# Kernel optimization log

Measured on AMD Instinct MI355X. Metric: run time of the kernel, lower is better.

## Reference

```python
import jax, jax.numpy as jnp
import numpy as np

B, C, D, H = 128, 8, 1024, 8
K_RANGE = (2, 3, 4, 5)


def setup_inputs() -> dict:
    key = jax.random.key(0)
    ks = jax.random.split(key, 10)
    s = 0.02
    return {
        "x": jax.random.normal(ks[0], (B, D), jnp.float32),
        # per-K prototype groups, shape (nb_classes, K, embed_dim) as in get_prototype_group()
        "p2": jax.random.normal(ks[1], (C, 2, D), jnp.float32),
        "p3": jax.random.normal(ks[2], (C, 3, D), jnp.float32),
        "p4": jax.random.normal(ks[3], (C, 4, D), jnp.float32),
        "p5": jax.random.normal(ks[4], (C, 5, D), jnp.float32),
        # per-class attention Block params (stacked over class axis)
        "ln_g": jnp.ones((C, D), jnp.float32),
        "ln_b": jnp.zeros((C, D), jnp.float32),
        "w_qkv": jax.random.normal(ks[5], (C, 3 * D, D), jnp.float32) * s,
        "b_qkv": jnp.zeros((C, 3 * D), jnp.float32),
        "w_proj": jax.random.normal(ks[6], (C, D, D), jnp.float32) * s,
        "b_proj": jnp.zeros((C, D), jnp.float32),
        # cls head
        "w_cls": jax.random.normal(ks[7], (C, D), jnp.float32) * s,
        "b_cls": jnp.zeros((C,), jnp.float32),
    }


def _proto_group(x, pg):
    """x: (B,D); pg: (C,K,D). Returns nearest proto (B,D), per-sample class group (B,K,D), class ids (B,)."""
    Cc, K, d = pg.shape
    flat = pg.reshape(Cc * K, d)
    # squared L2 distances (argmin identical to torch.cdist p=2 argmin)
    d2 = (jnp.sum(x * x, axis=1, keepdims=True)
          - 2.0 * (x @ flat.T)
          + jnp.sum(flat * flat, axis=1))
    idx = jnp.argmin(d2, axis=1)          # (B,)
    cls = idx // K                        # (B,)
    return flat[idx], pg[cls], cls


def _vicreg(x, nearest, proto_space, sim_c=25.0, std_c=25.0, cov_c=1.0):
    # sim: pull x toward its nearest prototype in every K-group
    repr_loss = jnp.mean((x[:, None, :] - nearest) ** 2)
    # std over batch of prototype space, unbiased var, eps=1e-4
    std = jnp.sqrt(jnp.var(proto_space, axis=0, ddof=1) + 1e-4)   # (S,D)
    std_loss = jnp.mean(jax.nn.relu(1.0 - std))
    # covariance of centered flattened prototype space
    ps = proto_space - jnp.mean(proto_space, axis=0)
    P = ps.reshape(-1, ps.shape[-1])                              # (B*S, D)
    cov = P.T @ P / (P.shape[0] - 1)
    cov_loss = ((cov ** 2).sum() - (jnp.diagonal(cov) ** 2).sum()) / ps.shape[-1]
    return sim_c * repr_loss + std_c * std_loss + cov_c * cov_loss


def _forward(x, p2, p3, p4, p5, ln_g, ln_b, w_qkv, b_qkv, w_proj, b_proj, w_cls, b_cls):
    groups = (p2, p3, p4, p5)
    nearest_list, space_list, cls = [], [], None
    for pg in groups:
        n, sp, cls = _proto_group(x, pg)   # cls kept from LAST group, as in torch code
        nearest_list.append(n)
        space_list.append(sp)
    nearest = jnp.stack(nearest_list, axis=1)     # (B, len(K_range), D)
    proto_space = jnp.concatenate(space_list, 1)  # (B, sum(K_range), D)

    vcr = _vicreg(x, nearest, proto_space)

    # per-class attention Block: LayerNorm -> MHA -> residual, vectorized over class axis c
    S = proto_space.shape[1]
    mu = proto_space.mean(-1, keepdims=True)
    var = proto_space.var(-1, keepdims=True)
    xn = (proto_space - mu) * jax.lax.rsqrt(var + 1e-5)               # (B,S,D)
    h = xn[None] * ln_g[:, None, None, :] + ln_b[:, None, None, :]    # (C,B,S,D)

    qkv = jnp.einsum('cbsd,cfd->cbsf', h, w_qkv) + b_qkv[:, None, None, :]
    dh = D // H
    qkv = qkv.reshape(C, B, S, 3, H, dh).transpose(3, 0, 1, 4, 2, 5)  # (3,C,B,H,S,dh)
    q, k, v = qkv[0] * (dh ** -0.5), qkv[1], qkv[2]
    attn = jax.nn.softmax(jnp.einsum('cbhqe,cbhke->cbhqk', q, k), axis=-1)
    o = jnp.einsum('cbhqk,cbhke->cbhqe', attn, v)                     # (C,B,H,S,dh)
    o = o.transpose(0, 1, 3, 2, 4).reshape(C, B, S, D)
    out = jnp.einsum('cbsd,ced->cbse', o, w_proj) + b_proj[:, None, None, :]
    attended = proto_space[None] + out                                # (C,B,S,D)

    # route each sample through the block of its (last-group) assigned class
    cond = attended[cls, jnp.arange(B)]                               # (B,S,D)
    cond = cond / jnp.maximum(jnp.linalg.norm(cond, axis=2, keepdims=True), 1e-12)
    pooled = cond.mean(1)                                             # (B,D)
    logits = pooled @ w_cls.T + b_cls
    return logits, vcr


def reference(x, p2, p3, p4, p5, ln_g, ln_b, w_qkv, b_qkv, w_proj, b_proj, w_cls, b_cls):
    return _forward(x, p2, p3, p4, p5, ln_g, ln_b, w_qkv, b_qkv, w_proj, b_proj, w_cls, b_cls)
```

## Files before the change

### kernel.cpp

```cpp
#include <hip/hip_runtime.h>
#include <math.h>

#define NB 128
#define ND 1024
#define NS 14
#define NDH 128

typedef float f32x4 __attribute__((ext_vector_type(4)));
typedef short bf16x8 __attribute__((ext_vector_type(8)));
typedef unsigned int u32x4 __attribute__((ext_vector_type(4)));

__device__ __forceinline__ unsigned short f2bf(float v) {
  unsigned int u = __builtin_bit_cast(unsigned int, v);
  return (unsigned short)((u + 0x7FFFu + ((u >> 16) & 1u)) >> 16);
}
__device__ __forceinline__ float bf2f(unsigned short u) {
  return __builtin_bit_cast(float, (unsigned int)u << 16);
}

__device__ __forceinline__ bf16x8 pack_bv(float4 w0, float4 w1) {
  unsigned int u0, u1, u2, u3;
  asm("v_cvt_pk_bf16_f32 %0, %1, %2" : "=v"(u0) : "v"(w0.x), "v"(w0.y));
  asm("v_cvt_pk_bf16_f32 %0, %1, %2" : "=v"(u1) : "v"(w0.z), "v"(w0.w));
  asm("v_cvt_pk_bf16_f32 %0, %1, %2" : "=v"(u2) : "v"(w1.x), "v"(w1.y));
  asm("v_cvt_pk_bf16_f32 %0, %1, %2" : "=v"(u3) : "v"(w1.z), "v"(w1.w));
  u32x4 u = {u0, u1, u2, u3};
  return __builtin_bit_cast(bf16x8, u);
}

__device__ __forceinline__ void s_decomp(int s, int& g, int& k) {
  if (s < 2)      { g = 0; k = s; }
  else if (s < 5) { g = 1; k = s - 2; }
  else if (s < 9) { g = 2; k = s - 5; }
  else            { g = 3; k = s - 9; }
}
__device__ __forceinline__ const float* grp_ptr(int g, const float* p2, const float* p3,
                                                const float* p4, const float* p5) {
  return g == 0 ? p2 : g == 1 ? p3 : g == 2 ? p4 : p5;
}
__device__ __forceinline__ int grp_base(int g) { return g == 0 ? 0 : g == 1 ? 16 : g == 2 ? 40 : 72; }
__device__ __forceinline__ int grp_k(int g) { return g + 2; }

__global__ __launch_bounds__(256) void k_ln(
    const float* __restrict__ p2, const float* __restrict__ p3,
    const float* __restrict__ p4, const float* __restrict__ p5,
    const float* __restrict__ ln_g, const float* __restrict__ ln_b,
    unsigned short* __restrict__ hbf2, float* __restrict__ pall)
{
  int r = blockIdx.x, t = threadIdx.x;
  __shared__ __align__(16) float xs[ND];
  float4* xs4 = (float4*)xs;
  const float* pp; int idx;
  if (r < 16)      { pp = p2; idx = r; }
  else if (r < 40) { pp = p3; idx = r - 16; }
  else if (r < 72) { pp = p4; idx = r - 40; }
  else             { pp = p5; idx = r - 72; }
  const float4* row4 = (const float4*)(pp + (size_t)idx * ND);
  float4 v = row4[t];
  xs4[t] = v;
  float s1 = v.x + v.y + v.z + v.w;
  float s2 = v.x * v.x + v.y * v.y + v.z * v.z + v.w * v.w;
  __shared__ float ra[256], rb[256];
  ra[t] = s1; rb[t] = s2; __syncthreads();
  for (int o = 128; o > 0; o >>= 1) { if (t < o) { ra[t] += ra[t + o]; rb[t] += rb[t + o]; } __syncthreads(); }
  __shared__ float mu, rstd;
  if (t == 0) {
    float m = ra[0] * (1.f / 1024.f);
    float var = rb[0] * (1.f / 1024.f) - m * m;
    mu = m; rstd = rsqrtf(var + 1e-5f);
  }
  __syncthreads();
  ((float4*)(pall + (size_t)r * ND))[t] = xs4[t];
  float4 xv = xs4[t];
  float nx = (xv.x - mu) * rstd, ny = (xv.y - mu) * rstd,
        nz = (xv.z - mu) * rstd, nw = (xv.w - mu) * rstd;
  int d0 = t * 4;
  int m = r >> 4, rr = r & 15;
  int kblk = d0 >> 5, qq = (d0 >> 3) & 3, e0 = d0 & 7;
  size_t fidx = (size_t)kblk * 3584 + m * 512 + (qq * 16 + rr) * 8 + e0;
#pragma unroll
  for (int c = 0; c < 8; ++c) {
    float4 g = ((const float4*)(ln_g + (size_t)c * ND))[t];
    float4 bb = ((const float4*)(ln_b + (size_t)c * ND))[t];
    ushort4 u;
    u.x = f2bf(nx * g.x + bb.x); u.y = f2bf(ny * g.y + bb.y);
    u.z = f2bf(nz * g.z + bb.z); u.w = f2bf(nw * g.w + bb.w);
    *(ushort4*)&hbf2[(size_t)c * 114688 + fidx] = u;
  }
}

__global__ __launch_bounds__(512) void k_qkv_assign(
    const unsigned short* __restrict__ hbf2, const float* __restrict__ w_qkv,
    const float* __restrict__ b_qkv, unsigned short* __restrict__ qkv_bf,
    const float* __restrict__ x,
    const float* __restrict__ p2, const float* __restrict__ p3,
    const float* __restrict__ p4, const float* __restrict__ p5,
    int* __restrict__ cls, int* __restrict__ rows_g, float* __restrict__ minv)
{
  __shared__ __align__(16) float lred[3 * 2 * 7 * 256];
  int bid = blockIdx.x, t = threadIdx.x;
  if (bid < 768) {
    int c = bid / 96, xb = bid - c * 96;
    int lane = t & 63, wid = t >> 6;
    int cg = wid & 1, ks = wid >> 1;
    int r16 = lane & 15, q = lane >> 4;
    int col = xb * 32 + cg * 16 + r16;
    const float* Wp = w_qkv + ((size_t)c * 3072 + col) * ND + ks * 256 + q * 8;
    const unsigned short* Hp = hbf2 + (size_t)c * 114688 + (size_t)(ks * 8) * 3584 + lane * 8;
    f32x4 acc[7] = {};
#pragma unroll
    for (int i = 0; i < 8; ++i) {
      float4 w0 = *(const float4*)(Wp + i * 32);
      float4 w1 = *(const float4*)(Wp + i * 32 + 4);
      bf16x8 bv = pack_bv(w0, w1);
      const unsigned short* hk = Hp + (size_t)i * 3584;
#pragma unroll
      for (int m = 0; m < 7; ++m) {
        bf16x8 av = *(const bf16x8*)(hk + m * 512);
        acc[m] = __builtin_amdgcn_mfma_f32_16x16x32_bf16(av, bv, acc[m], 0, 0, 0);
      }
    }
    if (ks) {
#pragma unroll
      for (int m = 0; m < 7; ++m)
        *(f32x4*)&lred[(((ks - 1) * 2 + cg) * 7 + m) * 256 + lane * 4] = acc[m];
    }
    __syncthreads();
    if (ks == 0) {
      float bq = b_qkv[(size_t)c * 3072 + col];
#pragma unroll
      for (int m = 0; m < 7; ++m) {
        f32x4 a1 = *(const f32x4*)&lred[((0 * 2 + cg) * 7 + m) * 256 + lane * 4];
        f32x4 a2 = *(const f32x4*)&lred[((1 * 2 + cg) * 7 + m) * 256 + lane * 4];
        f32x4 a3 = *(const f32x4*)&lred[((2 * 2 + cg) * 7 + m) * 256 + lane * 4];
#pragma unroll
        for (int r = 0; r < 4; ++r) {
          int row = m * 16 + q * 4 + r;
          qkv_bf[((size_t)c * 112 + row) * 3072 + col] = f2bf(acc[m][r] + a1[r] + a2[r] + a3[r] + bq);
        }
      }
    }
  } else {
    int b = bid - 768;
    float4* xs4 = (float4*)lred;
    float* d2s = lred + 1024;
    int* cls_s = (int*)(lred + 1152);
    if (t < 256) {
      const float4* xg4 = (const float4*)(x + (size_t)b * ND);
      xs4[t] = xg4[t];
    }
    __syncthreads();
    if (t < 112) {
      const float* pp; int idx;
      if (t < 16)      { pp = p2; idx = t; }
      else if (t < 40) { pp = p3; idx = t - 16; }
      else if (t < 72) { pp = p4; idx = t - 40; }
      else             { pp = p5; idx = t - 72; }
      const float4* pr4 = (const float4*)(pp + (size_t)idx * ND);
      float acc = 0.f;
#pragma unroll 8
      for (int d = 0; d < 256; ++d) {
        float4 a = xs4[d], p = pr4[d];
        float dx = a.x - p.x, dy = a.y - p.y, dz = a.z - p.z, dw = a.w - p.w;
        acc += dx * dx + dy * dy + dz * dz + dw * dw;
      }
      d2s[t] = acc;
    }
    __syncthreads();
    if (t < 4) {
      int base = grp_base(t), kg = grp_k(t), cnt = 8 * kg;
      float mv = d2s[base]; int mi = 0;
      for (int j = 1; j < cnt; ++j) { float v = d2s[base + j]; if (v < mv) { mv = v; mi = j; } }
      int c = mi / kg;
      cls[b * 4 + t] = c; cls_s[t] = c;
      minv[b * 4 + t] = mv;
    }
    __syncthreads();
    if (t < NS) {
      int g, k; s_decomp(t, g, k);
      rows_g[b * NS + t] = grp_base(g) + cls_s[g] * grp_k(g) + k;
    }
  }
}

__global__ __launch_bounds__(128) void k_prep(
    const int* __restrict__ cls, const float* __restrict__ minv,
    int* __restrict__ counts, int* __restrict__ ccnt, int* __restrict__ order,
    int* __restrict__ posof, int* __restrict__ chunkidx, int* __restrict__ chunk_c,
    int* __restrict__ chunk_lo, int* __restrict__ chunkN, float* __restrict__ scal)
{
  __shared__ int cnt_s[32];
  __shared__ int cc_s[8];
  __shared__ float red[128];
  int t = threadIdx.x;
  if (t < 32) cnt_s[t] = 0;
  if (t < 8) cc_s[t] = 0;
  if (t < 4) scal[t] = 0.f;
  __syncthreads();
  int c3;
#pragma unroll
  for (int g = 0; g < 4; ++g) {
    int c = cls[t * 4 + g];
    atomicAdd(&cnt_s[g * 8 + c], 1);
    if (g == 3) c3 = c;
  }
  int pos = atomicAdd(&cc_s[c3], 1);
  order[c3 * 128 + pos] = t;
  posof[t] = pos;
  red[t] = minv[t * 4 + 0] + minv[t * 4 + 1] + minv[t * 4 + 2] + minv[t * 4 + 3];
  __syncthreads();
  for (int o = 64; o > 0; o >>= 1) { if (t < o) red[t] += red[t + o]; __syncthreads(); }
  if (t == 0) {
    scal[0] = red[0];
    int T = 0;
    for (int c = 0; c < 8; ++c) {
      chunkidx[c] = T;
      int nch = (cc_s[c] + 15) >> 4;
      for (int j = 0; j < nch; ++j) { chunk_c[T] = c; chunk_lo[T] = j * 16; ++T; }
    }
    chunkN[0] = T;
  }
  if (t < 32) counts[t] = cnt_s[t];
  if (t < 8) ccnt[t] = cc_s[t];
}

__global__ __launch_bounds__(256) void k_attn_stats(
    const unsigned short* __restrict__ qkv_bf, const int* __restrict__ cls,
    const int* __restrict__ rows_g, const int* __restrict__ posof,
    const int* __restrict__ chunkidx, unsigned short* __restrict__ obf2,
    const float* __restrict__ p2, const float* __restrict__ p3,
    const float* __restrict__ p4, const float* __restrict__ p5,
    const int* __restrict__ counts, float* __restrict__ M, float* __restrict__ scal)
{
  int bid = blockIdx.x, t = threadIdx.x;
  if (bid < 1024) {
    __shared__ __align__(16) float qs[NS * NDH], ks2[NS * NDH], vs[NS * NDH];
    __shared__ float sc[NS * NS];
    __shared__ int rg[NS];
    int h = bid & 7, b = bid >> 3;
    if (t < NS) rg[t] = rows_g[b * NS + t];
    __syncthreads();
    int cp = cls[b * 4 + 3];
    int pos = posof[b];
    size_t gbase = (size_t)(chunkidx[cp] + (pos >> 4)) * 229376;
    int slot = pos & 15;
    const float scale = 0.08838834764831843f;
    for (int i = t; i < NS * 32; i += 256) {
      int s = i >> 5, e4 = (i & 31) * 4;
      size_t base = ((size_t)cp * 112 + rg[s]) * 3072 + h * NDH + e4;
      ushort4 uq = *(const ushort4*)&qkv_bf[base];
      ushort4 uk = *(const ushort4*)&qkv_bf[base + 1024];
      ushort4 uv = *(const ushort4*)&qkv_bf[base + 2048];
      int o = s * NDH + e4;
      qs[o]     = bf2f(uq.x) * scale; qs[o + 1] = bf2f(uq.y) * scale;
      qs[o + 2] = bf2f(uq.z) * scale; qs[o + 3] = bf2f(uq.w) * scale;
      ks2[o]     = bf2f(uk.x); ks2[o + 1] = bf2f(uk.y);
      ks2[o + 2] = bf2f(uk.z); ks2[o + 3] = bf2f(uk.w);
      vs[o]     = bf2f(uv.x); vs[o + 1] = bf2f(uv.y);
      vs[o + 2] = bf2f(uv.z); vs[o + 3] = bf2f(uv.w);
    }
    __syncthreads();
    if (t < NS * NS) {
      int si = t / NS, sj = t - (t / NS) * NS;
      const float4* qa = (const float4*)&qs[si * NDH];
      const float4* kb = (const float4*)&ks2[sj * NDH];
      float acc = 0.f;
#pragma unroll 8
      for (int e4 = 0; e4 < 32; ++e4) {
        float4 a = qa[e4], k4 = kb[e4];
        acc += a.x * k4.x + a.y * k4.y + a.z * k4.z + a.w * k4.w;
      }
      sc[t] = acc;
    }
    __syncthreads();
    if (t < NS) {
      float mx = -1e30f;
      for (int j = 0; j < NS; ++j) mx = fmaxf(mx, sc[t * NS + j]);
      float e_[NS]; float sum = 0.f;
      for (int j = 0; j < NS; ++j) { float e = expf(sc[t * NS + j] - mx); e_[j] = e; sum += e; }
      float inv = 1.f / sum;
      for (int j = 0; j < NS; ++j) sc[t * NS + j] = e_[j] * inv;
    }
    __syncthreads();
    for (int i = t; i < NS * 32; i += 256) {
      int s = i >> 5, e4 = i & 31;
      float4 a = {0.f, 0.f, 0.f, 0.f};
#pragma unroll
      for (int j = 0; j < NS; ++j) {
        float w = sc[s * NS + j];
        float4 v4 = ((const float4*)&vs[j * NDH])[e4];
        a.x += w * v4.x; a.y += w * v4.y; a.z += w * v4.z; a.w += w * v4.w;
      }
      int row = slot * 14 + s;
      int m = row >> 4, r16 = row & 15;
      int d0 = h * NDH + e4 * 4;
      int kblk = d0 >> 5, qq = (d0 >> 3) & 3, e0 = d0 & 7;
      ushort4 u; u.x = f2bf(a.x); u.y = f2bf(a.y); u.z = f2bf(a.z); u.w = f2bf(a.w);
      *(ushort4*)&obf2[gbase + (size_t)kblk * 7168 + m * 512 + (qq * 16 + r16) * 8 + e0] = u;
    }
  } else {
    int idx = (bid - 1024) * 256 + t;
    int s = idx >> 10, d = idx & 1023;
    int g, k; s_decomp(s, g, k);
    const float* pp = grp_ptr(g, p2, p3, p4, p5);
    int kg = grp_k(g);
    float vc[8], nc[8];
    float sum = 0.f, sumsq = 0.f;
#pragma unroll
    for (int c = 0; c < 8; ++c) {
      float v = pp[((size_t)(c * kg + k)) * ND + d];
      float n = (float)counts[g * 8 + c];
      vc[c] = v; nc[c] = n;
      sum += n * v; sumsq += n * v * v;
    }
    float mean = sum * (1.f / 128.f);
    float var = (sumsq - 128.f * mean * mean) * (1.f / 127.f);
    float sd = sqrtf(var + 1e-4f);
#pragma unroll
    for (int c = 0; c < 8; ++c)
      M[((size_t)(s * 8 + c)) * ND + d] = sqrtf(nc[c] * (1.f / 1791.f)) * (vc[c] - mean);
    float part = fmaxf(1.f - sd, 0.f);
    __shared__ float red[256];
    red[t] = part; __syncthreads();
    for (int o = 128; o > 0; o >>= 1) { if (t < o) red[t] += red[t + o]; __syncthreads(); }
    if (t == 0) atomicAdd(&scal[1], red[0]);
  }
}

__global__ __launch_bounds__(512) void k_proj_gram(
    const unsigned short* __restrict__ obf2, const int* __restrict__ order,
    const int* __restrict__ ccnt, const int* __restrict__ chunk_c,
    const int* __restrict__ chunk_lo, const int* __restrict__ chunkN,
    const int* __restrict__ rows_g,
    const float* __restrict__ w_proj, const float* __restrict__ b_proj,
    const float* __restrict__ pall, float* __restrict__ att,
    const float* __restrict__ M, float* __restrict__ scal)
{
  int bid = blockIdx.x, t = threadIdx.x;
  if (bid < 960) {
    int g = bid / 64, xb = bid - g * 64;
    if (g >= chunkN[0]) return;
    __shared__ __align__(16) float lred[3 * 2 * 7 * 256];
    __shared__ int sid_s[16];
    int c = chunk_c[g], lo = chunk_lo[g];
    int cnt = ccnt[c];
    int nb = cnt - lo; if (nb > 16) nb = 16;
    int lane = t & 63, wid = t >> 6;
    int rh = wid & 1, ks = wid >> 1;
    if (t < 16) sid_s[t] = order[c * 128 + lo + ((t < nb) ? t : nb - 1)];
    int r16 = lane & 15, q = lane >> 4;
    int col = xb * 16 + r16;
    const float* Wp = w_proj + ((size_t)c * ND + col) * ND + ks * 256 + q * 8;
    const unsigned short* Ap = obf2 + (size_t)g * 229376 + (size_t)(ks * 8) * 7168 + rh * 3584 + lane * 8;
    f32x4 acc[7] = {};
#pragma unroll
    for (int i = 0; i < 8; ++i) {
      float4 w0 = *(const float4*)(Wp + i * 32);
      float4 w1 = *(const float4*)(Wp + i * 32 + 4);
      bf16x8 bv = pack_bv(w0, w1);
      const unsigned short* ak = Ap + (size_t)i * 7168;
#pragma unroll
      for (int m = 0; m < 7; ++m) {
        bf16x8 av = *(const bf16x8*)(ak + m * 512);
        acc[m] = __builtin_amdgcn_mfma_f32_16x16x32_bf16(av, bv, acc[m], 0, 0, 0);
      }
    }
    if (ks) {
#pragma unroll
      for (int m = 0; m < 7; ++m)
        *(f32x4*)&lred[(((ks - 1) * 2 + rh) * 7 + m) * 256 + lane * 4] = acc[m];
    }
    __syncthreads();
    if (ks == 0) {
      float bp = b_proj[(size_t)c * ND + col];
#pragma unroll
      for (int m = 0; m < 7; ++m) {
        f32x4 a1 = *(const f32x4*)&lred[((0 * 2 + rh) * 7 + m) * 256 + lane * 4];
        f32x4 a2 = *(const f32x4*)&lred[((1 * 2 + rh) * 7 + m) * 256 + lane * 4];
        f32x4 a3 = *(const f32x4*)&lred[((2 * 2 + rh) * 7 + m) * 256 + lane * 4];
#pragma unroll
        for (int r = 0; r < 4; ++r) {
          int row = rh * 112 + m * 16 + q * 4 + r;
          int slot = row / 14, s = row - slot * 14;
          if (slot < nb) {
            int b = sid_s[slot];
            float res = pall[(size_t)rows_g[b * NS + s] * ND + col];
            att[((size_t)b * NS + s) * ND + col] = acc[m][r] + a1[r] + a2[r] + a3[r] + bp + res;
          }
        }
      }
    }
  } else if (bid < 1072) {
    int r = bid - 960;
    __shared__ __align__(16) float mi[ND];
    __shared__ float red2[128];
    float4* mi4 = (float4*)mi;
    const float4* src4 = (const float4*)(M + (size_t)r * ND);
    if (t < 256) mi4[t] = src4[t];
    if (t < 128) red2[t] = 0.f;
    __syncthreads();
    int j = t >> 2, qd = t & 3;
    float p = 0.f;
    if (j < 112) {
      const float4* mj4 = (const float4*)(M + (size_t)j * ND);
      float acc = 0.f;
#pragma unroll 8
      for (int d = qd * 64; d < qd * 64 + 64; ++d) {
        float4 a = mi4[d], b = mj4[d];
        acc += a.x * b.x + a.y * b.y + a.z * b.z + a.w * b.w;
      }
      acc += __shfl_xor(acc, 1, 4);
      acc += __shfl_xor(acc, 2, 4);
      p = acc * acc;
    }
    if (qd == 0 && j < 112) red2[j] = p;
    __syncthreads();
    for (int o = 64; o > 0; o >>= 1) { if (t < o) red2[t] += red2[t + o]; __syncthreads(); }
    if (t == 0) atomicAdd(&scal[2], red2[0]);
  } else {
    int d = (bid - 1072) * 512 + t;
    float tsum = 0.f;
    for (int r = 0; r < 112; ++r) { float v = M[(size_t)r * ND + d]; tsum += v * v; }
    __shared__ float red3[512];
    red3[t] = tsum * tsum; __syncthreads();
    for (int o = 256; o > 0; o >>= 1) { if (t < o) red3[t] += red3[t + o]; __syncthreads(); }
    if (t == 0) atomicAdd(&scal[3], red3[0]);
  }
}

__global__ __launch_bounds__(256) void k_final(
    const float* __restrict__ att, const float* __restrict__ w_cls,
    const float* __restrict__ b_cls, const float* __restrict__ scal,
    float* __restrict__ out)
{
  int b = blockIdx.x, t = threadIdx.x;
  __shared__ __align__(16) float as[NS * ND];
  __shared__ float wred[NS][4];
  __shared__ float inv[NS];
  __shared__ __align__(16) float pooled[ND];
  int lane = t & 63, w = t >> 6;
#pragma unroll
  for (int s = 0; s < NS; ++s) {
    float4 v = ((const float4*)(att + ((size_t)b * NS + s) * ND))[t];
    ((float4*)&as[s * ND])[t] = v;
    float p = v.x * v.x + v.y * v.y + v.z * v.z + v.w * v.w;
#pragma unroll
    for (int o = 32; o > 0; o >>= 1) p += __shfl_xor(p, o, 64);
    if (lane == 0) wred[s][w] = p;
  }
  __syncthreads();
  if (t < NS) {
    float s2 = wred[t][0] + wred[t][1] + wred[t][2] + wred[t][3];
    inv[t] = 1.f / fmaxf(sqrtf(s2), 1e-12f);
  }
  __syncthreads();
  float4 pa = {0.f, 0.f, 0.f, 0.f};
#pragma unroll
  for (int s = 0; s < NS; ++s) {
    float iv = inv[s];
    float4 v = ((const float4*)&as[s * ND])[t];
    pa.x += iv * v.x; pa.y += iv * v.y; pa.z += iv * v.z; pa.w += iv * v.w;
  }
  const float k14 = 1.f / 14.f;
  pa.x *= k14; pa.y *= k14; pa.z *= k14; pa.w *= k14;
  ((float4*)pooled)[t] = pa;
  __syncthreads();
  int c = t >> 5, l = t & 31;
  float acc = 0.f;
#pragma unroll
  for (int k = 0; k < 8; ++k) {
    int i4 = l + k * 32;
    float4 p4 = ((const float4*)pooled)[i4];
    float4 wc = ((const float4*)(w_cls + (size_t)c * ND))[i4];
    acc += p4.x * wc.x + p4.y * wc.y + p4.z * wc.z + p4.w * wc.w;
  }
  for (int o = 16; o > 0; o >>= 1) acc += __shfl_down(acc, o, 32);
  if (l == 0) out[b * 8 + c] = acc + b_cls[c];
  if (b == 0 && t == 0) {
    float repr = scal[0] * (1.f / (128.f * 4.f * 1024.f));
    float stdl = scal[1] * (1.f / 14336.f);
    float covl = (scal[2] - scal[3]) * (1.f / 1024.f);
    out[1024] = 25.f * repr + 25.f * stdl + covl;
  }
}

extern "C" void kernel_launch(void* const* d_in, const int* in_sizes, int n_in,
                              void* d_out, int out_size, void* d_ws, size_t ws_size,
                              hipStream_t stream) {
  const float* x      = (const float*)d_in[0];
  const float* p2     = (const float*)d_in[1];
  const float* p3     = (const float*)d_in[2];
  const float* p4     = (const float*)d_in[3];
  const float* p5     = (const float*)d_in[4];
  const float* ln_g   = (const float*)d_in[5];
  const float* ln_b   = (const float*)d_in[6];
  const float* w_qkv  = (const float*)d_in[7];
  const float* b_qkv  = (const float*)d_in[8];
  const float* w_proj = (const float*)d_in[9];
  const float* b_proj = (const float*)d_in[10];
  const float* w_cls  = (const float*)d_in[11];
  const float* b_cls  = (const float*)d_in[12];
  float* out = (float*)d_out;
  char* ws = (char*)d_ws;

  float* scal      = (float*)(ws + 0);
  int*   counts    = (int*)(ws + 64);
  int*   ccnt      = (int*)(ws + 192);
  int*   cls       = (int*)(ws + 256);
  int*   rows_g    = (int*)(ws + 2304);
  int*   order     = (int*)(ws + 9472);
  float* minv      = (float*)(ws + 13568);
  int*   posof     = (int*)(ws + 15616);
  int*   chunkidx  = (int*)(ws + 16128);
  int*   chunk_c   = (int*)(ws + 16160);
  int*   chunk_lo  = (int*)(ws + 16224);
  int*   chunkN    = (int*)(ws + 16288);
  float* pall      = (float*)(ws + 16384);
  unsigned short* hbf2 = (unsigned short*)(ws + 475136);
  unsigned short* qkvb = (unsigned short*)(ws + 2310144);
  unsigned short* obf2 = (unsigned short*)(ws + 7815168);
  float* att       = (float*)(ws + 15155200);
  float* M         = (float*)(ws + 22495232);

  k_ln<<<112, 256, 0, stream>>>(p2, p3, p4, p5, ln_g, ln_b, hbf2, pall);
  k_qkv_assign<<<896, 512, 0, stream>>>(hbf2, w_qkv, b_qkv, qkvb,
                                        x, p2, p3, p4, p5, cls, rows_g, minv);
  k_prep<<<1, 128, 0, stream>>>(cls, minv, counts, ccnt, order, posof, chunkidx, chunk_c, chunk_lo, chunkN, scal);
  k_attn_stats<<<1080, 256, 0, stream>>>(qkvb, cls, rows_g, posof, chunkidx, obf2,
                                         p2, p3, p4, p5, counts, M, scal);
  k_proj_gram<<<1074, 512, 0, stream>>>(obf2, order, ccnt, chunk_c, chunk_lo, chunkN, rows_g,
                                        w_proj, b_proj, pall, att, M, scal);
  k_final<<<128, 256, 0, stream>>>(att, w_cls, b_cls, scal, out);
}
```

Before: 124.0 us.

## Regroup stages into fewer kernels, halve GEMM blocks, prefetch MFMA operands

```diff
diff --git a/kernel.cpp b/kernel.cpp
--- a/kernel.cpp
+++ b/kernel.cpp
@@ -41,136 +41,87 @@
 __device__ __forceinline__ int grp_base(int g) { return g == 0 ? 0 : g == 1 ? 16 : g == 2 ? 40 : 72; }
 __device__ __forceinline__ int grp_k(int g) { return g + 2; }
 
-__global__ __launch_bounds__(256) void k_ln(
+__global__ __launch_bounds__(256) void k_ln_assign(
+    const float* __restrict__ x,
     const float* __restrict__ p2, const float* __restrict__ p3,
     const float* __restrict__ p4, const float* __restrict__ p5,
     const float* __restrict__ ln_g, const float* __restrict__ ln_b,
-    unsigned short* __restrict__ hbf2, float* __restrict__ pall)
+    unsigned short* __restrict__ hbf2, float* __restrict__ pall,
+    int* __restrict__ cls, int* __restrict__ rows_g, float* __restrict__ minv)
 {
-  int r = blockIdx.x, t = threadIdx.x;
+  int bid = blockIdx.x, t = threadIdx.x;
   __shared__ __align__(16) float xs[ND];
   float4* xs4 = (float4*)xs;
-  const float* pp; int idx;
-  if (r < 16)      { pp = p2; idx = r; }
-  else if (r < 40) { pp = p3; idx = r - 16; }
-  else if (r < 72) { pp = p4; idx = r - 40; }
-  else             { pp = p5; idx = r - 72; }
-  const float4* row4 = (const float4*)(pp + (size_t)idx * ND);
-  float4 v = row4[t];
-  xs4[t] = v;
-  float s1 = v.x + v.y + v.z + v.w;
-  float s2 = v.x * v.x + v.y * v.y + v.z * v.z + v.w * v.w;
-  __shared__ float ra[256], rb[256];
-  ra[t] = s1; rb[t] = s2; __syncthreads();
-  for (int o = 128; o > 0; o >>= 1) { if (t < o) { ra[t] += ra[t + o]; rb[t] += rb[t + o]; } __syncthreads(); }
-  __shared__ float mu, rstd;
-  if (t == 0) {
-    float m = ra[0] * (1.f / 1024.f);
-    float var = rb[0] * (1.f / 1024.f) - m * m;
-    mu = m; rstd = rsqrtf(var + 1e-5f);
-  }
-  __syncthreads();
-  ((float4*)(pall + (size_t)r * ND))[t] = xs4[t];
-  float4 xv = xs4[t];
-  float nx = (xv.x - mu) * rstd, ny = (xv.y - mu) * rstd,
-        nz = (xv.z - mu) * rstd, nw = (xv.w - mu) * rstd;
-  int d0 = t * 4;
-  int m = r >> 4, rr = r & 15;
-  int kblk = d0 >> 5, qq = (d0 >> 3) & 3, e0 = d0 & 7;
-  size_t fidx = (size_t)kblk * 3584 + m * 512 + (qq * 16 + rr) * 8 + e0;
-#pragma unroll
-  for (int c = 0; c < 8; ++c) {
-    float4 g = ((const float4*)(ln_g + (size_t)c * ND))[t];
-    float4 bb = ((const float4*)(ln_b + (size_t)c * ND))[t];
-    ushort4 u;
-    u.x = f2bf(nx * g.x + bb.x); u.y = f2bf(ny * g.y + bb.y);
-    u.z = f2bf(nz * g.z + bb.z); u.w = f2bf(nw * g.w + bb.w);
-    *(ushort4*)&hbf2[(size_t)c * 114688 + fidx] = u;
-  }
-}
-
-__global__ __launch_bounds__(512) void k_qkv_assign(
-    const unsigned short* __restrict__ hbf2, const float* __restrict__ w_qkv,
-    const float* __restrict__ b_qkv, unsigned short* __restrict__ qkv_bf,
-    const float* __restrict__ x,
-    const float* __restrict__ p2, const float* __restrict__ p3,
-    const float* __restrict__ p4, const float* __restrict__ p5,
-    int* __restrict__ cls, int* __restrict__ rows_g, float* __restrict__ minv)
-{
-  __shared__ __align__(16) float lred[3 * 2 * 7 * 256];
-  int bid = blockIdx.x, t = threadIdx.x;
-  if (bid < 768) {
-    int c = bid / 96, xb = bid - c * 96;
-    int lane = t & 63, wid = t >> 6;
-    int cg = wid & 1, ks = wid >> 1;
-    int r16 = lane & 15, q = lane >> 4;
-    int col = xb * 32 + cg * 16 + r16;
-    const float* Wp = w_qkv + ((size_t)c * 3072 + col) * ND + ks * 256 + q * 8;
-    const unsigned short* Hp = hbf2 + (size_t)c * 114688 + (size_t)(ks * 8) * 3584 + lane * 8;
-    f32x4 acc[7] = {};
-#pragma unroll
-    for (int i = 0; i < 8; ++i) {
-      float4 w0 = *(const float4*)(Wp + i * 32);
-      float4 w1 = *(const float4*)(Wp + i * 32 + 4);
-      bf16x8 bv = pack_bv(w0, w1);
-      const unsigned short* hk = Hp + (size_t)i * 3584;
-#pragma unroll
-      for (int m = 0; m < 7; ++m) {
-        bf16x8 av = *(const bf16x8*)(hk + m * 512);
-        acc[m] = __builtin_amdgcn_mfma_f32_16x16x32_bf16(av, bv, acc[m], 0, 0, 0);
-      }
-    }
-    if (ks) {
-#pragma unroll
-      for (int m = 0; m < 7; ++m)
-        *(f32x4*)&lred[(((ks - 1) * 2 + cg) * 7 + m) * 256 + lane * 4] = acc[m];
-    }
-    __syncthreads();
-    if (ks == 0) {
-      float bq = b_qkv[(size_t)c * 3072 + col];
-#pragma unroll
-      for (int m = 0; m < 7; ++m) {
-        f32x4 a1 = *(const f32x4*)&lred[((0 * 2 + cg) * 7 + m) * 256 + lane * 4];
-        f32x4 a2 = *(const f32x4*)&lred[((1 * 2 + cg) * 7 + m) * 256 + lane * 4];
-        f32x4 a3 = *(const f32x4*)&lred[((2 * 2 + cg) * 7 + m) * 256 + lane * 4];
-#pragma unroll
-        for (int r = 0; r < 4; ++r) {
-          int row = m * 16 + q * 4 + r;
-          qkv_bf[((size_t)c * 112 + row) * 3072 + col] = f2bf(acc[m][r] + a1[r] + a2[r] + a3[r] + bq);
-        }
-      }
+  if (bid < 112) {
+    int r = bid;
+    const float* pp; int idx;
+    if (r < 16)      { pp = p2; idx = r; }
+    else if (r < 40) { pp = p3; idx = r - 16; }
+    else if (r < 72) { pp = p4; idx = r - 40; }
+    else             { pp = p5; idx = r - 72; }
+    const float4* row4 = (const float4*)(pp + (size_t)idx * ND);
+    float4 v = row4[t];
+    xs4[t] = v;
+    float s1 = v.x + v.y + v.z + v.w;
+    float s2 = v.x * v.x + v.y * v.y + v.z * v.z + v.w * v.w;
+    __shared__ float ra[256], rb[256];
+    ra[t] = s1; rb[t] = s2; __syncthreads();
+    for (int o = 128; o > 0; o >>= 1) { if (t < o) { ra[t] += ra[t + o]; rb[t] += rb[t + o]; } __syncthreads(); }
+    __shared__ float mu, rstd;
+    if (t == 0) {
+      float m = ra[0] * (1.f / 1024.f);
+      float var = rb[0] * (1.f / 1024.f) - m * m;
+      mu = m; rstd = rsqrtf(var + 1e-5f);
+    }
+    __syncthreads();
+    ((float4*)(pall + (size_t)r * ND))[t] = xs4[t];
+    float4 xv = xs4[t];
+    float nx = (xv.x - mu) * rstd, ny = (xv.y - mu) * rstd,
+          nz = (xv.z - mu) * rstd, nw = (xv.w - mu) * rstd;
+    int d0 = t * 4;
+    int m = r >> 4, rr = r & 15;
+    int kblk = d0 >> 5, qq = (d0 >> 3) & 3, e0 = d0 & 7;
+    size_t fidx = (size_t)kblk * 3584 + m * 512 + (qq * 16 + rr) * 8 + e0;
+#pragma unroll
+    for (int c = 0; c < 8; ++c) {
+      float4 g = ((const float4*)(ln_g + (size_t)c * ND))[t];
+      float4 bb = ((const float4*)(ln_b + (size_t)c * ND))[t];
+      ushort4 u;
+      u.x = f2bf(nx * g.x + bb.x); u.y = f2bf(ny * g.y + bb.y);
+      u.z = f2bf(nz * g.z + bb.z); u.w = f2bf(nw * g.w + bb.w);
+      *(ushort4*)&hbf2[(size_t)c * 114688 + fidx] = u;
     }
   } else {
-    int b = bid - 768;
-    float4* xs4 = (float4*)lred;
-    float* d2s = lred + 1024;
-    int* cls_s = (int*)(lred + 1152);
-    if (t < 256) {
-      const float4* xg4 = (const float4*)(x + (size_t)b * ND);
-      xs4[t] = xg4[t];
-    }
-    __syncthreads();
-    if (t < 112) {
+    int b = bid - 112;
+    __shared__ float d2s[112];
+    __shared__ int cls_s[4];
+    const float4* xg4 = (const float4*)(x + (size_t)b * ND);
+    xs4[t] = xg4[t];
+    __syncthreads();
+    int j = t >> 1, half = t & 1;
+    if (j < 112) {
       const float* pp; int idx;
-      if (t < 16)      { pp = p2; idx = t; }
-      else if (t < 40) { pp = p3; idx = t - 16; }
-      else if (t < 72) { pp = p4; idx = t - 40; }
-      else             { pp = p5; idx = t - 72; }
+      if (j < 16)      { pp = p2; idx = j; }
+      else if (j < 40) { pp = p3; idx = j - 16; }
+      else if (j < 72) { pp = p4; idx = j - 40; }
+      else             { pp = p5; idx = j - 72; }
       const float4* pr4 = (const float4*)(pp + (size_t)idx * ND);
       float acc = 0.f;
+      int d0 = half * 128;
 #pragma unroll 8
-      for (int d = 0; d < 256; ++d) {
+      for (int d = d0; d < d0 + 128; ++d) {
         float4 a = xs4[d], p = pr4[d];
         float dx = a.x - p.x, dy = a.y - p.y, dz = a.z - p.z, dw = a.w - p.w;
         acc += dx * dx + dy * dy + dz * dz + dw * dw;
       }
-      d2s[t] = acc;
+      acc += __shfl_xor(acc, 1, 2);
+      if (half == 0) d2s[j] = acc;
     }
     __syncthreads();
     if (t < 4) {
       int base = grp_base(t), kg = grp_k(t), cnt = 8 * kg;
       float mv = d2s[base]; int mi = 0;
-      for (int j = 1; j < cnt; ++j) { float v = d2s[base + j]; if (v < mv) { mv = v; mi = j; } }
+      for (int jj = 1; jj < cnt; ++jj) { float v = d2s[base + jj]; if (v < mv) { mv = v; mi = jj; } }
       int c = mi / kg;
       cls[b * 4 + t] = c; cls_s[t] = c;
       minv[b * 4 + t] = mv;
@@ -183,45 +134,105 @@
   }
 }
 
-__global__ __launch_bounds__(128) void k_prep(
+__global__ __launch_bounds__(256, 4) void k_qkv_prep(
+    const unsigned short* __restrict__ hbf2, const float* __restrict__ w_qkv,
+    const float* __restrict__ b_qkv, unsigned short* __restrict__ qkv_bf,
     const int* __restrict__ cls, const float* __restrict__ minv,
     int* __restrict__ counts, int* __restrict__ ccnt, int* __restrict__ order,
     int* __restrict__ posof, int* __restrict__ chunkidx, int* __restrict__ chunk_c,
     int* __restrict__ chunk_lo, int* __restrict__ chunkN, float* __restrict__ scal)
 {
-  __shared__ int cnt_s[32];
-  __shared__ int cc_s[8];
-  __shared__ float red[128];
-  int t = threadIdx.x;
-  if (t < 32) cnt_s[t] = 0;
-  if (t < 8) cc_s[t] = 0;
-  if (t < 4) scal[t] = 0.f;
+  int bid = blockIdx.x, t = threadIdx.x;
+  if (bid == 0) {
+    __shared__ int cnt_s[32];
+    __shared__ int cc_s[8];
+    __shared__ float red[128];
+    if (t < 32) cnt_s[t] = 0;
+    if (t < 8) cc_s[t] = 0;
+    if (t < 4) scal[t] = 0.f;
+    __syncthreads();
+    if (t < 128) {
+      int c3;
+#pragma unroll
+      for (int g = 0; g < 4; ++g) {
+        int c = cls[t * 4 + g];
+        atomicAdd(&cnt_s[g * 8 + c], 1);
+        if (g == 3) c3 = c;
+      }
+      int pos = atomicAdd(&cc_s[c3], 1);
+      order[c3 * 128 + pos] = t;
+      posof[t] = pos;
+      red[t] = minv[t * 4 + 0] + minv[t * 4 + 1] + minv[t * 4 + 2] + minv[t * 4 + 3];
+    }
+    __syncthreads();
+    for (int o = 64; o > 0; o >>= 1) { if (t < o) red[t] += red[t + o]; __syncthreads(); }
+    if (t == 0) {
+      scal[0] = red[0];
+      int T = 0;
+      for (int c = 0; c < 8; ++c) {
+        chunkidx[c] = T;
+        int nch = (cc_s[c] + 15) >> 4;
+        for (int j = 0; j < nch; ++j) { chunk_c[T] = c; chunk_lo[T] = j * 16; ++T; }
+      }
+      chunkN[0] = T;
+    }
+    if (t < 32) counts[t] = cnt_s[t];
+    if (t < 8) ccnt[t] = cc_s[t];
+    return;
+  }
+  __shared__ __align__(16) float lred[3 * 7 * 256];
+  int qb = bid - 1;
+  int c = qb / 192, xb = qb - c * 192;
+  int lane = t & 63, ks = t >> 6;
+  int r16 = lane & 15, q = lane >> 4;
+  int col = xb * 16 + r16;
+  const float* Wp = w_qkv + ((size_t)c * 3072 + col) * ND + ks * 256 + q * 8;
+  const unsigned short* Hp = hbf2 + (size_t)c * 114688 + (size_t)(ks * 8) * 3584 + lane * 8;
+  f32x4 acc[7] = {};
+  float4 w0 = *(const float4*)(Wp);
+  float4 w1 = *(const float4*)(Wp + 4);
+  bf16x8 av[7];
+#pragma unroll
+  for (int m = 0; m < 7; ++m) av[m] = *(const bf16x8*)(Hp + m * 512);
+#pragma unroll
+  for (int i = 0; i < 8; ++i) {
+    float4 nw0, nw1; bf16x8 nav[7];
+    if (i < 7) {
+      nw0 = *(const float4*)(Wp + (i + 1) * 32);
+      nw1 = *(const float4*)(Wp + (i + 1) * 32 + 4);
+#pragma unroll
+      for (int m = 0; m < 7; ++m) nav[m] = *(const bf16x8*)(Hp + (size_t)(i + 1) * 3584 + m * 512);
+    }
+    bf16x8 bv = pack_bv(w0, w1);
+#pragma unroll
+    for (int m = 0; m < 7; ++m)
+      acc[m] = __builtin_amdgcn_mfma_f32_16x16x32_bf16(av[m], bv, acc[m], 0, 0, 0);
+    if (i < 7) {
+      w0 = nw0; w1 = nw1;
+#pragma unroll
+      for (int m = 0; m < 7; ++m) av[m] = nav[m];
+    }
+  }
+  if (ks) {
+#pragma unroll
+    for (int m = 0; m < 7; ++m)
+      *(f32x4*)&lred[((ks - 1) * 7 + m) * 256 + lane * 4] = acc[m];
+  }
   __syncthreads();
-  int c3;
-#pragma unroll
-  for (int g = 0; g < 4; ++g) {
-    int c = cls[t * 4 + g];
-    atomicAdd(&cnt_s[g * 8 + c], 1);
-    if (g == 3) c3 = c;
-  }
-  int pos = atomicAdd(&cc_s[c3], 1);
-  order[c3 * 128 + pos] = t;
-  posof[t] = pos;
-  red[t] = minv[t * 4 + 0] + minv[t * 4 + 1] + minv[t * 4 + 2] + minv[t * 4 + 3];
-  __syncthreads();
-  for (int o = 64; o > 0; o >>= 1) { if (t < o) red[t] += red[t + o]; __syncthreads(); }
-  if (t == 0) {
-    scal[0] = red[0];
-    int T = 0;
-    for (int c = 0; c < 8; ++c) {
-      chunkidx[c] = T;
-      int nch = (cc_s[c] + 15) >> 4;
-      for (int j = 0; j < nch; ++j) { chunk_c[T] = c; chunk_lo[T] = j * 16; ++T; }
-    }
-    chunkN[0] = T;
-  }
-  if (t < 32) counts[t] = cnt_s[t];
-  if (t < 8) ccnt[t] = cc_s[t];
+  if (ks == 0) {
+    float bq = b_qkv[(size_t)c * 3072 + col];
+#pragma unroll
+    for (int m = 0; m < 7; ++m) {
+      f32x4 a1 = *(const f32x4*)&lred[(0 * 7 + m) * 256 + lane * 4];
+      f32x4 a2 = *(const f32x4*)&lred[(1 * 7 + m) * 256 + lane * 4];
+      f32x4 a3 = *(const f32x4*)&lred[(2 * 7 + m) * 256 + lane * 4];
+#pragma unroll
+      for (int r = 0; r < 4; ++r) {
+        int row = m * 16 + q * 4 + r;
+        qkv_bf[((size_t)c * 112 + row) * 3072 + col] = f2bf(acc[m][r] + a1[r] + a2[r] + a3[r] + bq);
+      }
+    }
+  }
 }
 
 __global__ __launch_bounds__(256) void k_attn_stats(
@@ -327,7 +338,7 @@
   }
 }
 
-__global__ __launch_bounds__(512) void k_proj_gram(
+__global__ __launch_bounds__(256, 4) void k_proj_gram(
     const unsigned short* __restrict__ obf2, const int* __restrict__ order,
     const int* __restrict__ ccnt, const int* __restrict__ chunk_c,
     const int* __restrict__ chunk_lo, const int* __restrict__ chunkN,
@@ -337,47 +348,60 @@
     const float* __restrict__ M, float* __restrict__ scal)
 {
   int bid = blockIdx.x, t = threadIdx.x;
-  if (bid < 960) {
-    int g = bid / 64, xb = bid - g * 64;
+  if (bid < 2048) {
+    int xb = bid & 63;
+    int grh = bid >> 6;
+    int rh = grh & 1, g = grh >> 1;
     if (g >= chunkN[0]) return;
-    __shared__ __align__(16) float lred[3 * 2 * 7 * 256];
+    __shared__ __align__(16) float lred[3 * 7 * 256];
     __shared__ int sid_s[16];
     int c = chunk_c[g], lo = chunk_lo[g];
     int cnt = ccnt[c];
     int nb = cnt - lo; if (nb > 16) nb = 16;
-    int lane = t & 63, wid = t >> 6;
-    int rh = wid & 1, ks = wid >> 1;
+    int lane = t & 63, ks = t >> 6;
     if (t < 16) sid_s[t] = order[c * 128 + lo + ((t < nb) ? t : nb - 1)];
     int r16 = lane & 15, q = lane >> 4;
     int col = xb * 16 + r16;
     const float* Wp = w_proj + ((size_t)c * ND + col) * ND + ks * 256 + q * 8;
     const unsigned short* Ap = obf2 + (size_t)g * 229376 + (size_t)(ks * 8) * 7168 + rh * 3584 + lane * 8;
     f32x4 acc[7] = {};
+    float4 w0 = *(const float4*)(Wp);
+    float4 w1 = *(const float4*)(Wp + 4);
+    bf16x8 av[7];
+#pragma unroll
+    for (int m = 0; m < 7; ++m) av[m] = *(const bf16x8*)(Ap + m * 512);
 #pragma unroll
     for (int i = 0; i < 8; ++i) {
-      float4 w0 = *(const float4*)(Wp + i * 32);
-      float4 w1 = *(const float4*)(Wp + i * 32 + 4);
+      float4 nw0, nw1; bf16x8 nav[7];
+      if (i < 7) {
+        nw0 = *(const float4*)(Wp + (i + 1) * 32);
+        nw1 = *(const float4*)(Wp + (i + 1) * 32 + 4);
+#pragma unroll
+        for (int m = 0; m < 7; ++m) nav[m] = *(const bf16x8*)(Ap + (size_t)(i + 1) * 7168 + m * 512);
+      }
       bf16x8 bv = pack_bv(w0, w1);
-      const unsigned short* ak = Ap + (size_t)i * 7168;
-#pragma unroll
-      for (int m = 0; m < 7; ++m) {
-        bf16x8 av = *(const bf16x8*)(ak + m * 512);
-        acc[m] = __builtin_amdgcn_mfma_f32_16x16x32_bf16(av, bv, acc[m], 0, 0, 0);
+#pragma unroll
+      for (int m = 0; m < 7; ++m)
+        acc[m] = __builtin_amdgcn_mfma_f32_16x16x32_bf16(av[m], bv, acc[m], 0, 0, 0);
+      if (i < 7) {
+        w0 = nw0; w1 = nw1;
+#pragma unroll
+        for (int m = 0; m < 7; ++m) av[m] = nav[m];
       }
     }
     if (ks) {
 #pragma unroll
       for (int m = 0; m < 7; ++m)
-        *(f32x4*)&lred[(((ks - 1) * 2 + rh) * 7 + m) * 256 + lane * 4] = acc[m];
+        *(f32x4*)&lred[((ks - 1) * 7 + m) * 256 + lane * 4] = acc[m];
     }
     __syncthreads();
     if (ks == 0) {
       float bp = b_proj[(size_t)c * ND + col];
 #pragma unroll
       for (int m = 0; m < 7; ++m) {
-        f32x4 a1 = *(const f32x4*)&lred[((0 * 2 + rh) * 7 + m) * 256 + lane * 4];
-        f32x4 a2 = *(const f32x4*)&lred[((1 * 2 + rh) * 7 + m) * 256 + lane * 4];
-        f32x4 a3 = *(const f32x4*)&lred[((2 * 2 + rh) * 7 + m) * 256 + lane * 4];
+        f32x4 a1 = *(const f32x4*)&lred[(0 * 7 + m) * 256 + lane * 4];
+        f32x4 a2 = *(const f32x4*)&lred[(1 * 7 + m) * 256 + lane * 4];
+        f32x4 a3 = *(const f32x4*)&lred[(2 * 7 + m) * 256 + lane * 4];
 #pragma unroll
         for (int r = 0; r < 4; ++r) {
           int row = rh * 112 + m * 16 + q * 4 + r;
@@ -390,40 +414,38 @@
         }
       }
     }
-  } else if (bid < 1072) {
-    int r = bid - 960;
+  } else if (bid < 2160) {
+    int r = bid - 2048;
     __shared__ __align__(16) float mi[ND];
     __shared__ float red2[128];
     float4* mi4 = (float4*)mi;
     const float4* src4 = (const float4*)(M + (size_t)r * ND);
-    if (t < 256) mi4[t] = src4[t];
+    mi4[t] = src4[t];
     if (t < 128) red2[t] = 0.f;
     __syncthreads();
-    int j = t >> 2, qd = t & 3;
-    float p = 0.f;
+    int j = t >> 1, half = t & 1;
     if (j < 112) {
       const float4* mj4 = (const float4*)(M + (size_t)j * ND);
       float acc = 0.f;
+      int d0 = half * 128;
 #pragma unroll 8
-      for (int d = qd * 64; d < qd * 64 + 64; ++d) {
+      for (int d = d0; d < d0 + 128; ++d) {
         float4 a = mi4[d], b = mj4[d];
         acc += a.x * b.x + a.y * b.y + a.z * b.z + a.w * b.w;
       }
-      acc += __shfl_xor(acc, 1, 4);
-      acc += __shfl_xor(acc, 2, 4);
-      p = acc * acc;
-    }
-    if (qd == 0 && j < 112) red2[j] = p;
+      acc += __shfl_xor(acc, 1, 2);
+      if (half == 0) red2[j] = acc * acc;
+    }
     __syncthreads();
     for (int o = 64; o > 0; o >>= 1) { if (t < o) red2[t] += red2[t + o]; __syncthreads(); }
     if (t == 0) atomicAdd(&scal[2], red2[0]);
   } else {
-    int d = (bid - 1072) * 512 + t;
+    int d = (bid - 2160) * 256 + t;
     float tsum = 0.f;
     for (int r = 0; r < 112; ++r) { float v = M[(size_t)r * ND + d]; tsum += v * v; }
-    __shared__ float red3[512];
+    __shared__ float red3[256];
     red3[t] = tsum * tsum; __syncthreads();
-    for (int o = 256; o > 0; o >>= 1) { if (t < o) red3[t] += red3[t + o]; __syncthreads(); }
+    for (int o = 128; o > 0; o >>= 1) { if (t < o) red3[t] += red3[t + o]; __syncthreads(); }
     if (t == 0) atomicAdd(&scal[3], red3[0]);
   }
 }
@@ -522,13 +544,12 @@
   float* att       = (float*)(ws + 15155200);
   float* M         = (float*)(ws + 22495232);
 
-  k_ln<<<112, 256, 0, stream>>>(p2, p3, p4, p5, ln_g, ln_b, hbf2, pall);
-  k_qkv_assign<<<896, 512, 0, stream>>>(hbf2, w_qkv, b_qkv, qkvb,
-                                        x, p2, p3, p4, p5, cls, rows_g, minv);
-  k_prep<<<1, 128, 0, stream>>>(cls, minv, counts, ccnt, order, posof, chunkidx, chunk_c, chunk_lo, chunkN, scal);
+  k_ln_assign<<<240, 256, 0, stream>>>(x, p2, p3, p4, p5, ln_g, ln_b, hbf2, pall, cls, rows_g, minv);
+  k_qkv_prep<<<1537, 256, 0, stream>>>(hbf2, w_qkv, b_qkv, qkvb, cls, minv,
+                                       counts, ccnt, order, posof, chunkidx, chunk_c, chunk_lo, chunkN, scal);
   k_attn_stats<<<1080, 256, 0, stream>>>(qkvb, cls, rows_g, posof, chunkidx, obf2,
                                          p2, p3, p4, p5, counts, M, scal);
-  k_proj_gram<<<1074, 512, 0, stream>>>(obf2, order, ccnt, chunk_c, chunk_lo, chunkN, rows_g,
+  k_proj_gram<<<2164, 256, 0, stream>>>(obf2, order, ccnt, chunk_c, chunk_lo, chunkN, rows_g,
                                         w_proj, b_proj, pall, att, M, scal);
   k_final<<<128, 256, 0, stream>>>(att, w_cls, b_cls, scal, out);
 }
```

After: 125.6 us. No clear change (+1.3%).
